# Kernel tuning notes

Hardware: AMD Instinct MI355X
Metric: run time of the kernel (lower is better)

## Reference

```python
import math
import jax, jax.numpy as jnp
import numpy as np

L = 4        # n_layer
H = 8        # n_head
C = 512      # n_embd
V = 50257    # vocab_size
BLK = 1024   # block_size
R = 8        # lora_rank
LORA_SCALING = 32.0 / 8.0  # lora_alpha / lora_rank
B, T = 2, 1024


def _layernorm(x, g, b, eps=1e-5):
    m = jnp.mean(x, axis=-1, keepdims=True)
    v = jnp.var(x, axis=-1, keepdims=True)
    return (x - m) / jnp.sqrt(v + eps) * g + b


def _new_gelu(x):
    # 0.5*x*(1+tanh(sqrt(2/pi)*(x+0.044715*x^3)))
    return 0.5 * x * (1.0 + jnp.tanh(math.sqrt(2.0 / math.pi) * (x + 0.044715 * x ** 3)))


def _lora_linear(x, W, A, Bm):
    # nn.Linear (no bias) + LoRA low-rank update (dropout is identity in eval)
    return x @ W.T + LORA_SCALING * ((x @ A.T) @ Bm.T)


def setup_inputs() -> dict:
    key = jax.random.key(0)
    ks = jax.random.split(key, 16)
    s = 0.02  # GPT-2 init std
    inp = {
        'idx': jax.random.randint(ks[0], (B, T), 0, V, dtype=jnp.int64),
        'wte': jax.random.normal(ks[1], (V, C), jnp.float32) * s,
        'wpe': jax.random.normal(ks[2], (BLK, C), jnp.float32) * s,
        'ln1_g': jnp.ones((L, C), jnp.float32),
        'ln1_b': jnp.zeros((L, C), jnp.float32),
        'attn_w': jax.random.normal(ks[3], (L, 3 * C, C), jnp.float32) * s,
        'attn_lA': jax.random.normal(ks[4], (L, R, C), jnp.float32) * s,
        'attn_lB': jax.random.normal(ks[5], (L, 3 * C, R), jnp.float32) * s,
        'proj_w': jax.random.normal(ks[6], (L, C, C), jnp.float32) * (s / math.sqrt(2 * L)),
        'proj_lA': jax.random.normal(ks[7], (L, R, C), jnp.float32) * s,
        'proj_lB': jax.random.normal(ks[8], (L, C, R), jnp.float32) * s,
        'ln2_g': jnp.ones((L, C), jnp.float32),
        'ln2_b': jnp.zeros((L, C), jnp.float32),
        'fc_w': jax.random.normal(ks[9], (L, 4 * C, C), jnp.float32) * s,
        'fc_b': jnp.zeros((L, 4 * C), jnp.float32),
        'mproj_w': jax.random.normal(ks[10], (L, C, 4 * C), jnp.float32) * (s / math.sqrt(2 * L)),
        'mproj_b': jnp.zeros((L, C), jnp.float32),
        'lnf_g': jnp.ones((C,), jnp.float32),
        'lnf_b': jnp.zeros((C,), jnp.float32),
        'head_w': jax.random.normal(ks[11], (V, C), jnp.float32) * s,
    }
    return inp


def _gpt_forward(idx, wte, wpe, ln1_g, ln1_b, attn_w, attn_lA, attn_lB,
                 proj_w, proj_lA, proj_lB, ln2_g, ln2_b, fc_w, fc_b,
                 mproj_w, mproj_b, lnf_g, lnf_b, head_w):
    Bsz, Tlen = idx.shape
    hd = C // H
    x = wte[idx] + wpe[:Tlen][None, :, :]          # [B,T,C]
    mask = jnp.tril(jnp.ones((Tlen, Tlen), bool))  # causal mask
    for i in range(L):
        # --- attention ---
        h = _layernorm(x, ln1_g[i], ln1_b[i])
        qkv = _lora_linear(h, attn_w[i], attn_lA[i], attn_lB[i])  # [B,T,3C]
        q, k, v = jnp.split(qkv, 3, axis=-1)
        q = q.reshape(Bsz, Tlen, H, hd).transpose(0, 2, 1, 3)  # bhtd
        k = k.reshape(Bsz, Tlen, H, hd).transpose(0, 2, 1, 3)
        v = v.reshape(Bsz, Tlen, H, hd).transpose(0, 2, 1, 3)
        att = jnp.einsum('bhqd,bhkd->bhqk', q, k) * (1.0 / math.sqrt(hd))
        att = jnp.where(mask, att, -jnp.inf)
        att = jax.nn.softmax(att, axis=-1)
        y = jnp.einsum('bhqk,bhkd->bhqd', att, v)
        y = y.transpose(0, 2, 1, 3).reshape(Bsz, Tlen, C)
        y = _lora_linear(y, proj_w[i], proj_lA[i], proj_lB[i])
        x = x + y
        # --- MLP ---
        h2 = _layernorm(x, ln2_g[i], ln2_b[i])
        m = _new_gelu(h2 @ fc_w[i].T + fc_b[i]) @ mproj_w[i].T + mproj_b[i]
        x = x + m
    x = _layernorm(x, lnf_g, lnf_b)
    return x @ head_w.T  # logits [B,T,V]


def reference(idx, wte, wpe, ln1_g, ln1_b, attn_w, attn_lA, attn_lB,
              proj_w, proj_lA, proj_lB, ln2_g, ln2_b, fc_w, fc_b,
              mproj_w, mproj_b, lnf_g, lnf_b, head_w):
    return _gpt_forward(idx, wte, wpe, ln1_g, ln1_b, attn_w, attn_lA, attn_lB,
                        proj_w, proj_lA, proj_lB, ln2_g, ln2_b, fc_w, fc_b,
                        mproj_w, mproj_b, lnf_g, lnf_b, head_w)
```

## Files before the change

### kernel.cpp

```cpp
#include <hip/hip_runtime.h>
#include <cstdint>
#include <cstddef>

#define NLAYER 4
#define CDIM   512
#define TLEN   1024
#define BSZ    2
#define MROWS  (BSZ * TLEN)
#define VOCAB  50257
#define NHEAD  8
#define HDIM   64
#define LORA_S 4.0f

typedef unsigned short ushort_t;
typedef __attribute__((ext_vector_type(8))) short  short8;
typedef __attribute__((ext_vector_type(8))) _Float16 half8;
typedef __attribute__((ext_vector_type(4))) float  f32x4;
typedef __attribute__((ext_vector_type(4))) unsigned short us4;

__device__ inline ushort_t f2bf(float f) {
  union { float f; unsigned u; } c; c.f = f;
  unsigned u = c.u;
  u += 0x7fffu + ((u >> 16) & 1u);
  return (ushort_t)(u >> 16);
}

__device__ inline ushort_t f2h(float f) {
  union { _Float16 h; ushort_t u; } c; c.h = (_Float16)f;
  return c.u;
}

__device__ inline void stage16(const ushort_t* g, ushort_t* lds) {
  __builtin_amdgcn_global_load_lds(
      (__attribute__((address_space(1))) unsigned int*)(g),
      (__attribute__((address_space(3))) unsigned int*)(lds),
      16, 0, 0);
}

__global__ __launch_bounds__(256) void gemm_bt(const ushort_t* __restrict__ A,
                                               const ushort_t* __restrict__ B,
                                               float* __restrict__ C,
                                               int M, int N, int K) {
  __shared__ ushort_t As[128 * 32];
  __shared__ ushort_t Bs[128 * 32];
  const int tid  = threadIdx.x;
  const int wave = tid >> 6, lane = tid & 63;
  const int m0 = blockIdx.y << 7;
  const int n0 = blockIdx.x << 7;
  const int wr = (wave >> 1) << 6;
  const int wc = (wave & 1) << 6;
  const int lr = lane & 15;
  const int kq = (lane >> 4) << 3;

  f32x4 acc[4][4];
#pragma unroll
  for (int i = 0; i < 4; ++i)
#pragma unroll
    for (int j = 0; j < 4; ++j) {
      acc[i][j][0] = 0.f; acc[i][j][1] = 0.f;
      acc[i][j][2] = 0.f; acc[i][j][3] = 0.f;
    }

  for (int k0 = 0; k0 < K; k0 += 32) {
    __syncthreads();
#pragma unroll
    for (int i = 0; i < 2; ++i) {
      int c = i * 256 + tid;
      int row = c >> 2, col = (c & 3) << 3;
      stage16(A + (size_t)(m0 + row) * K + k0 + col,
              As + ((i * 256 + (wave << 6)) << 3));
    }
#pragma unroll
    for (int i = 0; i < 2; ++i) {
      int c = i * 256 + tid;
      int row = c >> 2, col = (c & 3) << 3;
      int n = n0 + row; if (n > N - 1) n = N - 1;
      stage16(B + (size_t)n * K + k0 + col,
              Bs + ((i * 256 + (wave << 6)) << 3));
    }
    __syncthreads();

    short8 af[4], bf[4];
#pragma unroll
    for (int i = 0; i < 4; ++i)
      af[i] = *(const short8*)(As + (wr + i * 16 + lr) * 32 + kq);
#pragma unroll
    for (int j = 0; j < 4; ++j)
      bf[j] = *(const short8*)(Bs + (wc + j * 16 + lr) * 32 + kq);
#pragma unroll
    for (int i = 0; i < 4; ++i)
#pragma unroll
      for (int j = 0; j < 4; ++j)
        acc[i][j] = __builtin_amdgcn_mfma_f32_16x16x32_bf16(af[i], bf[j], acc[i][j], 0, 0, 0);
  }

  const int rq = (lane >> 4) << 2;
  const int cl = lane & 15;
#pragma unroll
  for (int i = 0; i < 4; ++i) {
    int mb = m0 + wr + i * 16 + rq;
#pragma unroll
    for (int j = 0; j < 4; ++j) {
      int col = n0 + wc + j * 16 + cl;
      if (col < N) {
        float* cp = C + (size_t)mb * N + col;
#pragma unroll
        for (int r = 0; r < 4; ++r) cp[(size_t)r * N] = acc[i][j][r];
      }
    }
  }
}

__global__ void conv_bf16(const float* __restrict__ in, ushort_t* __restrict__ out, long n) {
  long i = ((long)blockIdx.x * 256 + threadIdx.x) * 4;
  if (i < n) {
    float4 v = *(const float4*)(in + i);
    us4 o = { f2bf(v.x), f2bf(v.y), f2bf(v.z), f2bf(v.w) };
    *(us4*)(out + i) = o;
  }
}

__global__ void conv_lora(const float* __restrict__ W, const float* __restrict__ lA,
                          const float* __restrict__ lB, ushort_t* __restrict__ out,
                          int N, long total) {
  long i = (long)blockIdx.x * 256 + threadIdx.x;
  if (i >= total) return;
  long nk = (long)N * CDIM;
  int  l  = (int)(i / nk);
  long r  = i - (long)l * nk;
  int  n  = (int)(r >> 9);
  int  k  = (int)(r & 511);
  const float* lAp = lA + (long)l * 8 * CDIM;
  const float* lBp = lB + (long)l * N * 8;
  float acc = W[i];
#pragma unroll
  for (int j = 0; j < 8; ++j) acc += LORA_S * lBp[n * 8 + j] * lAp[j * CDIM + k];
  out[i] = f2bf(acc);
}

__global__ void embed_kernel(const int* __restrict__ idx, const float* __restrict__ wte,
                             const float* __restrict__ wpe, float* __restrict__ x) {
  int i = blockIdx.x * 256 + threadIdx.x;
  int m = i >> 9, c = i & 511;
  int t = m & (TLEN - 1);
  x[i] = wte[(size_t)idx[m] * CDIM + c] + wpe[(size_t)t * CDIM + c];
}

__global__ __launch_bounds__(256) void ln_kernel(const float* __restrict__ x,
                                                 const float* __restrict__ g,
                                                 const float* __restrict__ b,
                                                 ushort_t* __restrict__ out) {
  const int m = blockIdx.x, tid = threadIdx.x;
  const float2 v = ((const float2*)(x + (size_t)m * CDIM))[tid];
  float s = v.x + v.y, ss = v.x * v.x + v.y * v.y;
#pragma unroll
  for (int off = 32; off; off >>= 1) { s += __shfl_xor(s, off); ss += __shfl_xor(ss, off); }
  __shared__ float rs[4], rss[4];
  const int w = tid >> 6, lane = tid & 63;
  if (lane == 0) { rs[w] = s; rss[w] = ss; }
  __syncthreads();
  s  = rs[0] + rs[1] + rs[2] + rs[3];
  ss = rss[0] + rss[1] + rss[2] + rss[3];
  const float mean = s * (1.f / CDIM);
  const float var  = ss * (1.f / CDIM) - mean * mean;
  const float rstd = rsqrtf(var + 1e-5f);
  const int c = tid * 2;
  out[(size_t)m * CDIM + c]     = f2bf((v.x - mean) * rstd * g[c]     + b[c]);
  out[(size_t)m * CDIM + c + 1] = f2bf((v.y - mean) * rstd * g[c + 1] + b[c + 1]);
}

__global__ __launch_bounds__(256) void attn_mfma(const float* __restrict__ qkv,
                                                 ushort_t* __restrict__ ybf) {
  __shared__ ushort_t Ks[32 * 72];
  __shared__ ushort_t Vt[64 * 40];
  __shared__ ushort_t Pl[4 * 16 * 40];

  const int tid  = threadIdx.x;
  const int wave = tid >> 6, lane = tid & 63;
  const int lr   = lane & 15;
  const int quad = lane >> 4;
  const int kq   = quad << 3;
  const int t0   = blockIdx.x << 6;
  const int bh   = blockIdx.y;
  const int bb   = bh >> 3, hh = bh & 7;
  const int qb   = t0 + (wave << 4);
  const size_t RS = 3 * CDIM;

  half8 aq[2];
  {
    const float* qr = qkv + (size_t)(bb * TLEN + qb + lr) * RS + hh * 64 + kq;
#pragma unroll
    for (int c = 0; c < 2; ++c) {
      float4 f0 = *(const float4*)(qr + c * 32);
      float4 f1 = *(const float4*)(qr + c * 32 + 4);
      half8 v;
      v[0] = (_Float16)f0.x; v[1] = (_Float16)f0.y;
      v[2] = (_Float16)f0.z; v[3] = (_Float16)f0.w;
      v[4] = (_Float16)f1.x; v[5] = (_Float16)f1.y;
      v[6] = (_Float16)f1.z; v[7] = (_Float16)f1.w;
      aq[c] = v;
    }
  }

  f32x4 o[4];
#pragma unroll
  for (int dt = 0; dt < 4; ++dt) { o[dt][0] = 0.f; o[dt][1] = 0.f; o[dt][2] = 0.f; o[dt][3] = 0.f; }
  float m[4] = { -1e30f, -1e30f, -1e30f, -1e30f };
  float l[4] = { 0.f, 0.f, 0.f, 0.f };

  const int kk    = tid & 31;
  const int dbase = (tid >> 5) << 3;

  const int ntiles = (blockIdx.x + 1) << 1;
  for (int kb = 0; kb < ntiles; ++kb) {
    const int kbase = kb << 5;
    __syncthreads();
    {
      const float* kp = qkv + (size_t)(bb * TLEN + kbase + kk) * RS + CDIM + hh * 64 + dbase;
      float4 f0 = *(const float4*)kp;
      float4 f1 = *(const float4*)(kp + 4);
      half8 kv;
      kv[0] = (_Float16)f0.x; kv[1] = (_Float16)f0.y;
      kv[2] = (_Float16)f0.z; kv[3] = (_Float16)f0.w;
      kv[4] = (_Float16)f1.x; kv[5] = (_Float16)f1.y;
      kv[6] = (_Float16)f1.z; kv[7] = (_Float16)f1.w;
      *(half8*)(Ks + kk * 72 + dbase) = kv;
      const float* vp = kp + CDIM;
      float4 g0 = *(const float4*)vp;
      float4 g1 = *(const float4*)(vp + 4);
      ushort_t vb[8] = { f2h(g0.x), f2h(g0.y), f2h(g0.z), f2h(g0.w),
                         f2h(g1.x), f2h(g1.y), f2h(g1.z), f2h(g1.w) };
#pragma unroll
      for (int j = 0; j < 8; ++j) Vt[(dbase + j) * 40 + kk] = vb[j];
    }
    __syncthreads();

    if (kbase <= qb + 15) {
      f32x4 st[2];
#pragma unroll
      for (int kt = 0; kt < 2; ++kt) {
        half8 b0 = *(const half8*)(Ks + (kt * 16 + lr) * 72 + kq);
        half8 b1 = *(const half8*)(Ks + (kt * 16 + lr) * 72 + 32 + kq);
        f32x4 acc = { 0.f, 0.f, 0.f, 0.f };
        acc = __builtin_amdgcn_mfma_f32_16x16x32_f16(aq[0], b0, acc, 0, 0, 0);
        acc = __builtin_amdgcn_mfma_f32_16x16x32_f16(aq[1], b1, acc, 0, 0, 0);
        st[kt] = acc;
      }
      float corr[4];
#pragma unroll
      for (int r = 0; r < 4; ++r) {
        const int qrow = qb + quad * 4 + r;
#pragma unroll
        for (int kt = 0; kt < 2; ++kt) {
          const int kcol = kbase + kt * 16 + lr;
          float s = st[kt][r] * 0.125f;
          st[kt][r] = (kcol <= qrow) ? s : -1e30f;
        }
        float mx = fmaxf(st[0][r], st[1][r]);
#pragma unroll
        for (int off = 8; off; off >>= 1) mx = fmaxf(mx, __shfl_xor(mx, off));
        const float mnew = fmaxf(m[r], mx);
        corr[r] = __expf(m[r] - mnew);
        m[r] = mnew;
        float p0 = __expf(st[0][r] - mnew);
        float p1 = __expf(st[1][r] - mnew);
        st[0][r] = p0; st[1][r] = p1;
        float ps = p0 + p1;
#pragma unroll
        for (int off = 8; off; off >>= 1) ps += __shfl_xor(ps, off);
        l[r] = l[r] * corr[r] + ps;
      }
#pragma unroll
      for (int dt = 0; dt < 4; ++dt)
#pragma unroll
        for (int r = 0; r < 4; ++r) o[dt][r] *= corr[r];
      ushort_t* pw = Pl + wave * 640;
#pragma unroll
      for (int kt = 0; kt < 2; ++kt)
#pragma unroll
        for (int r = 0; r < 4; ++r)
          pw[(quad * 4 + r) * 40 + kt * 16 + lr] = f2h(st[kt][r]);
      half8 ap = *(const half8*)(pw + lr * 40 + kq);
#pragma unroll
      for (int dt = 0; dt < 4; ++dt) {
        half8 bv = *(const half8*)(Vt + (dt * 16 + lr) * 40 + kq);
        o[dt] = __builtin_amdgcn_mfma_f32_16x16x32_f16(ap, bv, o[dt], 0, 0, 0);
      }
    }
  }

#pragma unroll
  for (int r = 0; r < 4; ++r) {
    const float inv = 1.0f / l[r];
    const int qrow = qb + quad * 4 + r;
    ushort_t* yp = ybf + (size_t)(bb * TLEN + qrow) * CDIM + hh * 64;
#pragma unroll
    for (int dt = 0; dt < 4; ++dt)
      yp[dt * 16 + lr] = f2bf(o[dt][r] * inv);
  }
}

__global__ void add_res(float* __restrict__ x, const float* __restrict__ d,
                        const float* __restrict__ bias, int n) {
  int i = blockIdx.x * 256 + threadIdx.x;
  if (i < n) {
    float v = x[i] + d[i];
    if (bias) v += bias[i & 511];
    x[i] = v;
  }
}

__global__ void gelu_bias(const float* __restrict__ in, const float* __restrict__ bias,
                          ushort_t* __restrict__ out, int n) {
  int i = blockIdx.x * 256 + threadIdx.x;
  if (i < n) {
    float v = in[i] + bias[i & 2047];
    float t = tanhf(0.7978845608028654f * (v + 0.044715f * v * v * v));
    out[i] = f2bf(0.5f * v * (1.0f + t));
  }
}

extern "C" void kernel_launch(void* const* d_in, const int* in_sizes, int n_in,
                              void* d_out, int out_size, void* d_ws, size_t ws_size,
                              hipStream_t stream) {
  const int*   idx     = (const int*)  d_in[0];
  const float* wte     = (const float*)d_in[1];
  const float* wpe     = (const float*)d_in[2];
  const float* ln1_g   = (const float*)d_in[3];
  const float* ln1_b   = (const float*)d_in[4];
  const float* attn_w  = (const float*)d_in[5];
  const float* attn_lA = (const float*)d_in[6];
  const float* attn_lB = (const float*)d_in[7];
  const float* proj_w  = (const float*)d_in[8];
  const float* proj_lA = (const float*)d_in[9];
  const float* proj_lB = (const float*)d_in[10];
  const float* ln2_g   = (const float*)d_in[11];
  const float* ln2_b   = (const float*)d_in[12];
  const float* fc_w    = (const float*)d_in[13];
  const float* fc_b    = (const float*)d_in[14];
  const float* mproj_w = (const float*)d_in[15];
  const float* mproj_b = (const float*)d_in[16];
  const float* lnf_g   = (const float*)d_in[17];
  const float* lnf_b   = (const float*)d_in[18];
  const float* head_w  = (const float*)d_in[19];
  float* out = (float*)d_out;

  uintptr_t p = (uintptr_t)d_ws;
  auto take = [&](size_t bytes) -> void* {
    uintptr_t q = p;
    p = (p + bytes + 255) & ~(uintptr_t)255;
    return (void*)q;
  };
  ushort_t* wAttnB  = (ushort_t*)take((size_t)NLAYER * 1536 * 512 * 2);
  ushort_t* wProjB  = (ushort_t*)take((size_t)NLAYER * 512 * 512 * 2);
  ushort_t* wFcB    = (ushort_t*)take((size_t)NLAYER * 2048 * 512 * 2);
  ushort_t* wMprojB = (ushort_t*)take((size_t)NLAYER * 512 * 2048 * 2);
  ushort_t* wHeadB  = (ushort_t*)take((size_t)VOCAB * 512 * 2);
  float*    x       = (float*)   take((size_t)MROWS * 512 * 4);
  ushort_t* hbf     = (ushort_t*)take((size_t)MROWS * 512 * 2);
  float*    qkv     = (float*)   take((size_t)MROWS * 1536 * 4);
  ushort_t* ybf     = (ushort_t*)take((size_t)MROWS * 512 * 2);
  float*    tmp     = (float*)   take((size_t)MROWS * 512 * 4);
  float*    fcf     = (float*)   take((size_t)MROWS * 2048 * 4);
  ushort_t* mbf     = (ushort_t*)take((size_t)MROWS * 2048 * 2);

  {
    long nA = (long)NLAYER * 1536 * 512;
    conv_lora<<<(int)((nA + 255) / 256), 256, 0, stream>>>(attn_w, attn_lA, attn_lB, wAttnB, 1536, nA);
    long nP = (long)NLAYER * 512 * 512;
    conv_lora<<<(int)((nP + 255) / 256), 256, 0, stream>>>(proj_w, proj_lA, proj_lB, wProjB, 512, nP);
    long nF = (long)NLAYER * 2048 * 512;
    conv_bf16<<<(int)((nF / 4 + 255) / 256), 256, 0, stream>>>(fc_w, wFcB, nF);
    long nM = (long)NLAYER * 512 * 2048;
    conv_bf16<<<(int)((nM / 4 + 255) / 256), 256, 0, stream>>>(mproj_w, wMprojB, nM);
    long nH = (long)VOCAB * 512;
    conv_bf16<<<(int)((nH / 4 + 255) / 256), 256, 0, stream>>>(head_w, wHeadB, nH);
  }

  embed_kernel<<<(MROWS * 512) / 256, 256, 0, stream>>>(idx, wte, wpe, x);

  for (int l = 0; l < NLAYER; ++l) {
    ln_kernel<<<MROWS, 256, 0, stream>>>(x, ln1_g + l * 512, ln1_b + l * 512, hbf);
    gemm_bt<<<dim3(1536 / 128, MROWS / 128), 256, 0, stream>>>(
        hbf, wAttnB + (size_t)l * 1536 * 512, qkv, MROWS, 1536, 512);
    attn_mfma<<<dim3(TLEN / 64, BSZ * NHEAD), 256, 0, stream>>>(qkv, ybf);
    gemm_bt<<<dim3(512 / 128, MROWS / 128), 256, 0, stream>>>(
        ybf, wProjB + (size_t)l * 512 * 512, tmp, MROWS, 512, 512);
    add_res<<<(MROWS * 512) / 256, 256, 0, stream>>>(x, tmp, nullptr, MROWS * 512);

    ln_kernel<<<MROWS, 256, 0, stream>>>(x, ln2_g + l * 512, ln2_b + l * 512, hbf);
    gemm_bt<<<dim3(2048 / 128, MROWS / 128), 256, 0, stream>>>(
        hbf, wFcB + (size_t)l * 2048 * 512, fcf, MROWS, 2048, 512);
    gelu_bias<<<(MROWS * 2048) / 256, 256, 0, stream>>>(fcf, fc_b + l * 2048, mbf, MROWS * 2048);
    gemm_bt<<<dim3(512 / 128, MROWS / 128), 256, 0, stream>>>(
        mbf, wMprojB + (size_t)l * 512 * 2048, tmp, MROWS, 512, 2048);
    add_res<<<(MROWS * 512) / 256, 256, 0, stream>>>(x, tmp, mproj_b + l * 512, MROWS * 512);
  }

  ln_kernel<<<MROWS, 256, 0, stream>>>(x, lnf_g, lnf_b, hbf);
  gemm_bt<<<dim3((VOCAB + 127) / 128, MROWS / 128), 256, 0, stream>>>(
      hbf, wHeadB, out, MROWS, VOCAB, 512);
}
```

Measured before the change: 1.447 ms.

## Fuse GELU+bias into FC GEMM and residual add into 64-tile projection GEMMs

The FC GEMM gains a templated epilogue that adds the bias, applies GELU and writes bf16 directly, so the fp32 intermediate buffer and the separate gelu kernel are no longer needed. The attention and MLP output projections move to a new 64x64-tile GEMM that adds the result (plus bias) straight into the residual stream, which removes the tmp buffer and the add_res kernels. The smaller tiles give N=512 GEMMs more blocks to fill the GPU, at the cost of less data reuse per block.

```diff
diff --git a/kernel.cpp b/kernel.cpp
--- a/kernel.cpp
+++ b/kernel.cpp
@@ -30,6 +30,11 @@
   return c.u;
 }
 
+__device__ inline float gelu_f(float v) {
+  float t = tanhf(0.7978845608028654f * (v + 0.044715f * v * v * v));
+  return 0.5f * v * (1.0f + t);
+}
+
 __device__ inline void stage16(const ushort_t* g, ushort_t* lds) {
   __builtin_amdgcn_global_load_lds(
       (__attribute__((address_space(1))) unsigned int*)(g),
@@ -37,9 +42,11 @@
       16, 0, 0);
 }
 
+template<int EPI>
 __global__ __launch_bounds__(256) void gemm_bt(const ushort_t* __restrict__ A,
                                                const ushort_t* __restrict__ B,
-                                               float* __restrict__ C,
+                                               void* __restrict__ Cv,
+                                               const float* __restrict__ bias,
                                                int M, int N, int K) {
   __shared__ ushort_t As[128 * 32];
   __shared__ ushort_t Bs[128 * 32];
@@ -103,10 +110,80 @@
     for (int j = 0; j < 4; ++j) {
       int col = n0 + wc + j * 16 + cl;
       if (col < N) {
-        float* cp = C + (size_t)mb * N + col;
-#pragma unroll
-        for (int r = 0; r < 4; ++r) cp[(size_t)r * N] = acc[i][j][r];
+        if (EPI == 0) {
+          float* cp = (float*)Cv + (size_t)mb * N + col;
+#pragma unroll
+          for (int r = 0; r < 4; ++r) cp[(size_t)r * N] = acc[i][j][r];
+        } else {
+          ushort_t* cp = (ushort_t*)Cv + (size_t)mb * N + col;
+          const float bb = bias[col];
+#pragma unroll
+          for (int r = 0; r < 4; ++r) cp[(size_t)r * N] = f2bf(gelu_f(acc[i][j][r] + bb));
+        }
       }
+    }
+  }
+}
+
+__global__ __launch_bounds__(256) void gemm64_res(const ushort_t* __restrict__ A,
+                                                  const ushort_t* __restrict__ B,
+                                                  float* __restrict__ x,
+                                                  const float* __restrict__ bias,
+                                                  int M, int N, int K) {
+  __shared__ ushort_t As[64 * 32];
+  __shared__ ushort_t Bs[64 * 32];
+  const int tid  = threadIdx.x;
+  const int wave = tid >> 6, lane = tid & 63;
+  const int m0 = blockIdx.y << 6;
+  const int n0 = blockIdx.x << 6;
+  const int wr = (wave >> 1) << 5;
+  const int wc = (wave & 1) << 5;
+  const int lr = lane & 15;
+  const int kq = (lane >> 4) << 3;
+
+  f32x4 acc[2][2];
+#pragma unroll
+  for (int i = 0; i < 2; ++i)
+#pragma unroll
+    for (int j = 0; j < 2; ++j) {
+      acc[i][j][0] = 0.f; acc[i][j][1] = 0.f;
+      acc[i][j][2] = 0.f; acc[i][j][3] = 0.f;
+    }
+
+  const int row = tid >> 2, col = (tid & 3) << 3;
+
+  for (int k0 = 0; k0 < K; k0 += 32) {
+    __syncthreads();
+    stage16(A + (size_t)(m0 + row) * K + k0 + col, As + (wave << 9));
+    stage16(B + (size_t)(n0 + row) * K + k0 + col, Bs + (wave << 9));
+    __syncthreads();
+
+    short8 af[2], bf[2];
+#pragma unroll
+    for (int i = 0; i < 2; ++i)
+      af[i] = *(const short8*)(As + (wr + i * 16 + lr) * 32 + kq);
+#pragma unroll
+    for (int j = 0; j < 2; ++j)
+      bf[j] = *(const short8*)(Bs + (wc + j * 16 + lr) * 32 + kq);
+#pragma unroll
+    for (int i = 0; i < 2; ++i)
+#pragma unroll
+      for (int j = 0; j < 2; ++j)
+        acc[i][j] = __builtin_amdgcn_mfma_f32_16x16x32_bf16(af[i], bf[j], acc[i][j], 0, 0, 0);
+  }
+
+  const int rq = (lane >> 4) << 2;
+  const int cl = lane & 15;
+#pragma unroll
+  for (int i = 0; i < 2; ++i) {
+    int mb = m0 + wr + i * 16 + rq;
+#pragma unroll
+    for (int j = 0; j < 2; ++j) {
+      int c = n0 + wc + j * 16 + cl;
+      float bb = bias ? bias[c] : 0.f;
+      float* xp = x + (size_t)mb * N + c;
+#pragma unroll
+      for (int r = 0; r < 4; ++r) xp[(size_t)r * N] = xp[(size_t)r * N] + acc[i][j][r] + bb;
     }
   }
 }
@@ -297,26 +374,6 @@
 #pragma unroll
     for (int dt = 0; dt < 4; ++dt)
       yp[dt * 16 + lr] = f2bf(o[dt][r] * inv);
-  }
-}
-
-__global__ void add_res(float* __restrict__ x, const float* __restrict__ d,
-                        const float* __restrict__ bias, int n) {
-  int i = blockIdx.x * 256 + threadIdx.x;
-  if (i < n) {
-    float v = x[i] + d[i];
-    if (bias) v += bias[i & 511];
-    x[i] = v;
-  }
-}
-
-__global__ void gelu_bias(const float* __restrict__ in, const float* __restrict__ bias,
-                          ushort_t* __restrict__ out, int n) {
-  int i = blockIdx.x * 256 + threadIdx.x;
-  if (i < n) {
-    float v = in[i] + bias[i & 2047];
-    float t = tanhf(0.7978845608028654f * (v + 0.044715f * v * v * v));
-    out[i] = f2bf(0.5f * v * (1.0f + t));
   }
 }
 
@@ -360,8 +417,6 @@
   ushort_t* hbf     = (ushort_t*)take((size_t)MROWS * 512 * 2);
   float*    qkv     = (float*)   take((size_t)MROWS * 1536 * 4);
   ushort_t* ybf     = (ushort_t*)take((size_t)MROWS * 512 * 2);
-  float*    tmp     = (float*)   take((size_t)MROWS * 512 * 4);
-  float*    fcf     = (float*)   take((size_t)MROWS * 2048 * 4);
   ushort_t* mbf     = (ushort_t*)take((size_t)MROWS * 2048 * 2);
 
   {
@@ -381,23 +436,20 @@
 
   for (int l = 0; l < NLAYER; ++l) {
     ln_kernel<<<MROWS, 256, 0, stream>>>(x, ln1_g + l * 512, ln1_b + l * 512, hbf);
-    gemm_bt<<<dim3(1536 / 128, MROWS / 128), 256, 0, stream>>>(
-        hbf, wAttnB + (size_t)l * 1536 * 512, qkv, MROWS, 1536, 512);
+    gemm_bt<0><<<dim3(1536 / 128, MROWS / 128), 256, 0, stream>>>(
+        hbf, wAttnB + (size_t)l * 1536 * 512, qkv, nullptr, MROWS, 1536, 512);
     attn_mfma<<<dim3(TLEN / 64, BSZ * NHEAD), 256, 0, stream>>>(qkv, ybf);
-    gemm_bt<<<dim3(512 / 128, MROWS / 128), 256, 0, stream>>>(
-        ybf, wProjB + (size_t)l * 512 * 512, tmp, MROWS, 512, 512);
-    add_res<<<(MROWS * 512) / 256, 256, 0, stream>>>(x, tmp, nullptr, MROWS * 512);
+    gemm64_res<<<dim3(512 / 64, MROWS / 64), 256, 0, stream>>>(
+        ybf, wProjB + (size_t)l * 512 * 512, x, nullptr, MROWS, 512, 512);
 
     ln_kernel<<<MROWS, 256, 0, stream>>>(x, ln2_g + l * 512, ln2_b + l * 512, hbf);
-    gemm_bt<<<dim3(2048 / 128, MROWS / 128), 256, 0, stream>>>(
-        hbf, wFcB + (size_t)l * 2048 * 512, fcf, MROWS, 2048, 512);
-    gelu_bias<<<(MROWS * 2048) / 256, 256, 0, stream>>>(fcf, fc_b + l * 2048, mbf, MROWS * 2048);
-    gemm_bt<<<dim3(512 / 128, MROWS / 128), 256, 0, stream>>>(
-        mbf, wMprojB + (size_t)l * 512 * 2048, tmp, MROWS, 512, 2048);
-    add_res<<<(MROWS * 512) / 256, 256, 0, stream>>>(x, tmp, mproj_b + l * 512, MROWS * 512);
+    gemm_bt<2><<<dim3(2048 / 128, MROWS / 128), 256, 0, stream>>>(
+        hbf, wFcB + (size_t)l * 2048 * 512, mbf, fc_b + l * 2048, MROWS, 2048, 512);
+    gemm64_res<<<dim3(512 / 64, MROWS / 64), 256, 0, stream>>>(
+        mbf, wMprojB + (size_t)l * 512 * 2048, x, mproj_b + l * 512, MROWS, 512, 2048);
   }
 
   ln_kernel<<<MROWS, 256, 0, stream>>>(x, lnf_g, lnf_b, hbf);
-  gemm_bt<<<dim3((VOCAB + 127) / 128, MROWS / 128), 256, 0, stream>>>(
-      hbf, wHeadB, out, MROWS, VOCAB, 512);
-}
+  gemm_bt<0><<<dim3((VOCAB + 127) / 128, MROWS / 128), 256, 0, stream>>>(
+      hbf, wHeadB, out, nullptr, MROWS, VOCAB, 512);
+}
```

Result: faster. 1.337 ms (-7.6%).
